# Kernel tuning notes

Hardware: AMD Instinct MI355X
Metric: run time of the kernel (lower is better)

Reference implementation:

```python
import jax, jax.numpy as jnp
import numpy as np

N_NODES = 65536
N_EDGES = 524288
GRAPH_SIZE = 512  # equal-size graphs -> batch = arange(N)//512
N_GRAPHS = N_NODES // GRAPH_SIZE
IN_DIM, HID, OUT_DIM, HEADS = 64, 64, 128, 4


def setup_inputs() -> dict:
    key = jax.random.key(0)
    ks = jax.random.split(key, 24)
    s = 0.1  # init scale
    # within-graph random edges
    g = jax.random.randint(ks[0], (N_EDGES,), 0, N_GRAPHS)
    off = jax.random.randint(ks[1], (2, N_EDGES), 0, GRAPH_SIZE)
    edge_index = (g[None, :] * GRAPH_SIZE + off).astype(jnp.int32)
    batch = (jnp.arange(N_NODES) // GRAPH_SIZE).astype(jnp.int32)
    rn = lambda k, sh: jax.random.normal(k, sh, jnp.float32) * s
    return {
        'x': jax.random.normal(ks[2], (N_NODES, IN_DIM), jnp.float32),
        'edge_index': edge_index, 'batch': batch,
        'W1': rn(ks[3], (IN_DIM, HEADS * HID)), 'a1s': rn(ks[4], (HEADS, HID)),
        'a1d': rn(ks[5], (HEADS, HID)), 'b1': jnp.zeros((HEADS * HID,), jnp.float32),
        'W2': rn(ks[6], (HEADS * HID, HEADS * HID)), 'a2s': rn(ks[7], (HEADS, HID)),
        'a2d': rn(ks[8], (HEADS, HID)), 'b2': jnp.zeros((HEADS * HID,), jnp.float32),
        'W3': rn(ks[9], (HEADS * HID, OUT_DIM)), 'a3s': rn(ks[10], (1, OUT_DIM)),
        'a3d': rn(ks[11], (1, OUT_DIM)), 'b3': jnp.zeros((OUT_DIM,), jnp.float32),
        'g1': jnp.ones((HEADS * HID,), jnp.float32), 'be1': jnp.zeros((HEADS * HID,), jnp.float32),
        'g2': jnp.ones((HEADS * HID,), jnp.float32), 'be2': jnp.zeros((HEADS * HID,), jnp.float32),
        'Wr': rn(ks[12], (IN_DIM, OUT_DIM)), 'br': jnp.zeros((OUT_DIM,), jnp.float32),
        'Wq': rn(ks[13], (OUT_DIM, OUT_DIM)), 'Wk': rn(ks[14], (OUT_DIM, OUT_DIM)),
        'Wv': rn(ks[15], (OUT_DIM, OUT_DIM)), 'Wo': rn(ks[16], (OUT_DIM, OUT_DIM)),
        'bo': jnp.zeros((OUT_DIM,), jnp.float32),
    }


def _gat(x, src, dst, W, a_s, a_d, b, heads, out_ch):
    N = x.shape[0]
    h = (x @ W).reshape(N, heads, out_ch)          # [N,H,C]
    e_s = (h * a_s).sum(-1)                        # [N,H]
    e_d = (h * a_d).sum(-1)
    e = jax.nn.leaky_relu(e_s[src] + e_d[dst], 0.2)  # [E,H]
    m = jax.ops.segment_max(e, dst, num_segments=N)
    p = jnp.exp(e - m[dst])
    z = jax.ops.segment_sum(p, dst, num_segments=N)
    alpha = p / (z[dst] + 1e-16)
    out = jax.ops.segment_sum(alpha[:, :, None] * h[src], dst, num_segments=N)
    return out.reshape(N, heads * out_ch) + b


def _ln(x, g, b):
    mu = x.mean(-1, keepdims=True)
    v = ((x - mu) ** 2).mean(-1, keepdims=True)
    return (x - mu) * jax.lax.rsqrt(v + 1e-5) * g + b


def _mha(x, Wq, Wk, Wv, Wo, bo, heads):
    B, n, D = x.shape
    hd = D // heads
    q = (x @ Wq).reshape(B, n, heads, hd)
    k = (x @ Wk).reshape(B, n, heads, hd)
    v = (x @ Wv).reshape(B, n, heads, hd)
    energy = jnp.einsum('bqhd,bkhd->bhqk', q, k)
    att = jax.nn.softmax(energy / jnp.sqrt(jnp.float32(D)), axis=-1)
    out = jnp.einsum('bhqk,bkhd->bqhd', att, v).reshape(B, n, D)
    return out @ Wo + bo


def reference(x, edge_index, batch, W1, a1s, a1d, b1, W2, a2s, a2d, b2,
              W3, a3s, a3d, b3, g1, be1, g2, be2, Wr, br, Wq, Wk, Wv, Wo, bo):
    N = x.shape[0]
    loops = jnp.arange(N, dtype=edge_index.dtype)
    src = jnp.concatenate([edge_index[0], loops])  # PyG add_self_loops default
    dst = jnp.concatenate([edge_index[1], loops])
    h = jax.nn.elu(_gat(x, src, dst, W1, a1s, a1d, b1, HEADS, HID))
    h = _ln(h, g1, be1)
    h = jax.nn.elu(_gat(h, src, dst, W2, a2s, a2d, b2, HEADS, HID))
    h = _ln(h, g2, be2)
    h = _gat(h, src, dst, W3, a3s, a3d, b3, 1, OUT_DIM)
    h = h + (x @ Wr + br)
    # equal-size graphs: per-graph self-attention via batched reshape
    hg = h.reshape(N_GRAPHS, GRAPH_SIZE, OUT_DIM)
    hg = _mha(hg, Wq, Wk, Wv, Wo, bo, 4)
    return hg.reshape(N, OUT_DIM)
```

## Files before the change

kernel.cpp:

```cpp
#include <hip/hip_runtime.h>
#include <math.h>

#define N_NODES 65536
#define NUM_EDGES 524288
#define E_TOT   (NUM_EDGES + N_NODES)
#define GSZ 512

typedef _Float16 f16x8 __attribute__((ext_vector_type(8)));
typedef _Float16 f16x4 __attribute__((ext_vector_type(4)));
typedef _Float16 f16x2 __attribute__((ext_vector_type(2)));
typedef float    f32x16 __attribute__((ext_vector_type(16)));

__global__ void k_zero_int(int* __restrict__ p, int n) {
  int i = blockIdx.x * blockDim.x + threadIdx.x;
  if (i < n) p[i] = 0;
}

__global__ void k_hist(const int* __restrict__ ei, int* __restrict__ cnt) {
  int e = blockIdx.x * blockDim.x + threadIdx.x;
  if (e >= E_TOT) return;
  int dst = (e < NUM_EDGES) ? ei[NUM_EDGES + e] : (e - NUM_EDGES);
  atomicAdd(&cnt[dst], 1);
}

__global__ void k_scan1(const int* __restrict__ cnt, int* __restrict__ offs,
                        int* __restrict__ sums) {
  __shared__ int s[256];
  int t = threadIdx.x;
  int i = blockIdx.x * 256 + t;
  int v = cnt[i];
  s[t] = v;
  for (int o = 1; o < 256; o <<= 1) {
    __syncthreads();
    int x = (t >= o) ? s[t - o] : 0;
    __syncthreads();
    s[t] += x;
  }
  offs[i] = s[t] - v;
  if (t == 255) sums[blockIdx.x] = s[t];
}

__global__ void k_scan2(int* __restrict__ sums) {
  __shared__ int s[256];
  int t = threadIdx.x;
  int v = sums[t];
  s[t] = v;
  for (int o = 1; o < 256; o <<= 1) {
    __syncthreads();
    int x = (t >= o) ? s[t - o] : 0;
    __syncthreads();
    s[t] += x;
  }
  sums[t] = s[t] - v;
}

__global__ void k_scan3(int* __restrict__ offs, const int* __restrict__ sums,
                        int* __restrict__ cur) {
  int i = blockIdx.x * 256 + threadIdx.x;
  int v = offs[i] + sums[blockIdx.x];
  offs[i] = v;
  cur[i] = v;
  if (i == 0) offs[N_NODES] = E_TOT;
}

__global__ void k_fill(const int* __restrict__ ei, int* __restrict__ cur,
                       int* __restrict__ ssrc) {
  int e = blockIdx.x * blockDim.x + threadIdx.x;
  if (e >= E_TOT) return;
  int src, dst;
  if (e < NUM_EDGES) { src = ei[e]; dst = ei[NUM_EDGES + e]; }
  else               { src = e - NUM_EDGES; dst = src; }
  int pos = atomicAdd(&cur[dst], 1);
  ssrc[pos] = src;
}

__device__ __forceinline__ f16x8 cvt8(float4 a, float4 b) {
  f16x8 h;
  h[0] = (_Float16)a.x; h[1] = (_Float16)a.y;
  h[2] = (_Float16)a.z; h[3] = (_Float16)a.w;
  h[4] = (_Float16)b.x; h[5] = (_Float16)b.y;
  h[6] = (_Float16)b.z; h[7] = (_Float16)b.w;
  return h;
}

#define LDH 40
template <typename TA, typename TC>
__global__ __launch_bounds__(256) void k_gemm(
    const TA* __restrict__ A, const float* __restrict__ B,
    const float* __restrict__ bias, TC* __restrict__ C,
    int M, int N, int K, float cscale) {
  __shared__ __align__(16) _Float16 As[128][LDH];
  __shared__ __align__(16) _Float16 Bs[128][LDH];
  const int t = threadIdx.x;
  const int l = t & 63, w = t >> 6;
  const int m0 = blockIdx.x * 128, n0 = blockIdx.y * 128;
  const int wm = (w >> 1) * 64, wn = (w & 1) * 64;
  const int lm = l & 31, kq = l >> 5;

  f32x16 acc00 = {}, acc01 = {}, acc10 = {}, acc11 = {};

  const int ra = t >> 1, ka = (t & 1) << 4;
  const int nb = (t & 31) << 2, kb = (t >> 5) << 2;

  for (int k0 = 0; k0 < K; k0 += 32) {
    f16x8 a_lo, a_hi;
    if constexpr (sizeof(TA) == 4) {
      const float* ap = (const float*)&A[(size_t)(m0 + ra) * K + k0 + ka];
      float4 av0 = *(const float4*)ap;
      float4 av1 = *(const float4*)(ap + 4);
      float4 av2 = *(const float4*)(ap + 8);
      float4 av3 = *(const float4*)(ap + 12);
      a_lo = cvt8(av0, av1);
      a_hi = cvt8(av2, av3);
    } else {
      const _Float16* ap = (const _Float16*)&A[(size_t)(m0 + ra) * K + k0 + ka];
      a_lo = *(const f16x8*)ap;
      a_hi = *(const f16x8*)(ap + 8);
    }
    const float* bp = &B[(size_t)(k0 + kb) * N + n0 + nb];
    float4 bv0 = *(const float4*)bp;
    float4 bv1 = *(const float4*)(bp + N);
    float4 bv2 = *(const float4*)(bp + 2 * N);
    float4 bv3 = *(const float4*)(bp + 3 * N);
    __syncthreads();
    *(f16x8*)&As[ra][ka]     = a_lo;
    *(f16x8*)&As[ra][ka + 8] = a_hi;
    f16x4 g;
    g[0] = (_Float16)bv0.x; g[1] = (_Float16)bv1.x;
    g[2] = (_Float16)bv2.x; g[3] = (_Float16)bv3.x;
    *(f16x4*)&Bs[nb + 0][kb] = g;
    g[0] = (_Float16)bv0.y; g[1] = (_Float16)bv1.y;
    g[2] = (_Float16)bv2.y; g[3] = (_Float16)bv3.y;
    *(f16x4*)&Bs[nb + 1][kb] = g;
    g[0] = (_Float16)bv0.z; g[1] = (_Float16)bv1.z;
    g[2] = (_Float16)bv2.z; g[3] = (_Float16)bv3.z;
    *(f16x4*)&Bs[nb + 2][kb] = g;
    g[0] = (_Float16)bv0.w; g[1] = (_Float16)bv1.w;
    g[2] = (_Float16)bv2.w; g[3] = (_Float16)bv3.w;
    *(f16x4*)&Bs[nb + 3][kb] = g;
    __syncthreads();
#pragma unroll
    for (int ks = 0; ks < 2; ++ks) {
      f16x8 a0 = *(const f16x8*)&As[wm + lm][ks * 16 + kq * 8];
      f16x8 a1 = *(const f16x8*)&As[wm + 32 + lm][ks * 16 + kq * 8];
      f16x8 b0 = *(const f16x8*)&Bs[wn + lm][ks * 16 + kq * 8];
      f16x8 b1 = *(const f16x8*)&Bs[wn + 32 + lm][ks * 16 + kq * 8];
      acc00 = __builtin_amdgcn_mfma_f32_32x32x16_f16(a0, b0, acc00, 0, 0, 0);
      acc01 = __builtin_amdgcn_mfma_f32_32x32x16_f16(a0, b1, acc01, 0, 0, 0);
      acc10 = __builtin_amdgcn_mfma_f32_32x32x16_f16(a1, b0, acc10, 0, 0, 0);
      acc11 = __builtin_amdgcn_mfma_f32_32x32x16_f16(a1, b1, acc11, 0, 0, 0);
    }
  }

  const int cn = n0 + wn + lm;
  float b0v = 0.f, b1v = 0.f;
  if (bias) { b0v = bias[cn]; b1v = bias[cn + 32]; }
  const int rb = 4 * (l >> 5);
#pragma unroll
  for (int r = 0; r < 16; ++r) {
    int row = m0 + wm + (r & 3) + 8 * (r >> 2) + rb;
    C[(size_t)row * N + cn]             = (TC)((acc00[r] + b0v) * cscale);
    C[(size_t)row * N + cn + 32]        = (TC)((acc01[r] + b1v) * cscale);
    C[(size_t)(row + 32) * N + cn]      = (TC)((acc10[r] + b0v) * cscale);
    C[(size_t)(row + 32) * N + cn + 32] = (TC)((acc11[r] + b1v) * cscale);
  }
}

__global__ void k_scores(const _Float16* __restrict__ h, const float* __restrict__ as_,
                         const float* __restrict__ ad_, float* __restrict__ es,
                         float* __restrict__ ed, int H, int C) {
  int t = blockIdx.x * blockDim.x + threadIdx.x;
  if (t >= N_NODES * H) return;
  int hd = t % H;
  const _Float16* hp = h + (size_t)t * C;
  const float* ap = as_ + hd * C;
  const float* dp = ad_ + hd * C;
  float s = 0.f, d = 0.f;
  for (int c = 0; c < C; c += 8) {
    f16x8 hv = *(const f16x8*)&hp[c];
    float4 a0 = *(const float4*)&ap[c];
    float4 a1 = *(const float4*)&ap[c + 4];
    float4 d0 = *(const float4*)&dp[c];
    float4 d1 = *(const float4*)&dp[c + 4];
    float h0 = (float)hv[0], h1 = (float)hv[1], h2 = (float)hv[2], h3 = (float)hv[3];
    float h4 = (float)hv[4], h5 = (float)hv[5], h6 = (float)hv[6], h7 = (float)hv[7];
    s += h0 * a0.x + h1 * a0.y + h2 * a0.z + h3 * a0.w;
    s += h4 * a1.x + h5 * a1.y + h6 * a1.z + h7 * a1.w;
    d += h0 * d0.x + h1 * d0.y + h2 * d0.z + h3 * d0.w;
    d += h4 * d1.x + h5 * d1.y + h6 * d1.z + h7 * d1.w;
  }
  es[t] = s; ed[t] = d;
}

__device__ __forceinline__ float lrelu02(float e) { return e >= 0.f ? e : 0.2f * e; }

__global__ __launch_bounds__(256) void k_agg256(
    const _Float16* __restrict__ h, const float* __restrict__ es,
    const float* __restrict__ ed, const int* __restrict__ offs,
    const int* __restrict__ ssrc, const float* __restrict__ bias,
    const float* __restrict__ lng, const float* __restrict__ lnb,
    _Float16* __restrict__ out) {
  int lane = threadIdx.x & 63;
  int n = blockIdx.x * 4 + (threadIdx.x >> 6);
  int head = lane >> 4;
  int o0 = offs[n], deg = offs[n + 1] - o0;
  float4 edv = *(const float4*)&ed[n * 4];
  float edh = (head & 2) ? ((head & 1) ? edv.w : edv.z)
                         : ((head & 1) ? edv.y : edv.x);
  float m0 = -1e30f, m1 = -1e30f, m2 = -1e30f, m3 = -1e30f;
  for (int j = lane; j < deg; j += 64) {
    int s = ssrc[o0 + j];
    float4 ev = *(const float4*)&es[s * 4];
    m0 = fmaxf(m0, lrelu02(ev.x + edv.x));
    m1 = fmaxf(m1, lrelu02(ev.y + edv.y));
    m2 = fmaxf(m2, lrelu02(ev.z + edv.z));
    m3 = fmaxf(m3, lrelu02(ev.w + edv.w));
  }
#pragma unroll
  for (int o = 1; o < 64; o <<= 1) {
    m0 = fmaxf(m0, __shfl_xor(m0, o));
    m1 = fmaxf(m1, __shfl_xor(m1, o));
    m2 = fmaxf(m2, __shfl_xor(m2, o));
    m3 = fmaxf(m3, __shfl_xor(m3, o));
  }
  float mh = (head & 2) ? ((head & 1) ? m3 : m2) : ((head & 1) ? m1 : m0);
  float z = 0.f, a0 = 0.f, a1 = 0.f, a2 = 0.f, a3 = 0.f;
  int c0 = lane * 4;
  for (int j = 0; j < deg; ++j) {
    int s = ssrc[o0 + j];
    float p = __expf(lrelu02(es[s * 4 + head] + edh) - mh);
    z += p;
    f16x4 hv = *(const f16x4*)&h[(size_t)s * 256 + c0];
    a0 += p * (float)hv[0]; a1 += p * (float)hv[1];
    a2 += p * (float)hv[2]; a3 += p * (float)hv[3];
  }
  float inv = 1.f / (z + 1e-16f);
  float4 bv = *(const float4*)&bias[c0];
  float v0 = a0 * inv + bv.x; v0 = v0 > 0.f ? v0 : __expf(v0) - 1.f;
  float v1 = a1 * inv + bv.y; v1 = v1 > 0.f ? v1 : __expf(v1) - 1.f;
  float v2 = a2 * inv + bv.z; v2 = v2 > 0.f ? v2 : __expf(v2) - 1.f;
  float v3 = a3 * inv + bv.w; v3 = v3 > 0.f ? v3 : __expf(v3) - 1.f;
  float sum = v0 + v1 + v2 + v3;
#pragma unroll
  for (int o = 1; o < 64; o <<= 1) sum += __shfl_xor(sum, o);
  float mean = sum * (1.f / 256.f);
  float d0 = v0 - mean, d1 = v1 - mean, d2 = v2 - mean, d3 = v3 - mean;
  float sq = d0 * d0 + d1 * d1 + d2 * d2 + d3 * d3;
#pragma unroll
  for (int o = 1; o < 64; o <<= 1) sq += __shfl_xor(sq, o);
  float rs = rsqrtf(sq * (1.f / 256.f) + 1e-5f);
  float4 gv = *(const float4*)&lng[c0];
  float4 ev2 = *(const float4*)&lnb[c0];
  f16x4 o4;
  o4[0] = (_Float16)(d0 * rs * gv.x + ev2.x);
  o4[1] = (_Float16)(d1 * rs * gv.y + ev2.y);
  o4[2] = (_Float16)(d2 * rs * gv.z + ev2.z);
  o4[3] = (_Float16)(d3 * rs * gv.w + ev2.w);
  *(f16x4*)&out[(size_t)n * 256 + c0] = o4;
}

__global__ __launch_bounds__(256) void k_agg128(
    const _Float16* __restrict__ h, const float* __restrict__ es,
    const float* __restrict__ ed, const int* __restrict__ offs,
    const int* __restrict__ ssrc, const float* __restrict__ bias,
    float* __restrict__ io) {
  int lane = threadIdx.x & 63;
  int n = blockIdx.x * 4 + (threadIdx.x >> 6);
  int o0 = offs[n], deg = offs[n + 1] - o0;
  float edv = ed[n];
  float mx = -1e30f;
  for (int j = lane; j < deg; j += 64) {
    int s = ssrc[o0 + j];
    mx = fmaxf(mx, lrelu02(es[s] + edv));
  }
#pragma unroll
  for (int o = 1; o < 64; o <<= 1) mx = fmaxf(mx, __shfl_xor(mx, o));
  float z = 0.f, a0 = 0.f, a1 = 0.f;
  int c0 = lane * 2;
  for (int j = 0; j < deg; ++j) {
    int s = ssrc[o0 + j];
    float p = __expf(lrelu02(es[s] + edv) - mx);
    z += p;
    f16x2 hv = *(const f16x2*)&h[(size_t)s * 128 + c0];
    a0 += p * (float)hv[0]; a1 += p * (float)hv[1];
  }
  float inv = 1.f / (z + 1e-16f);
  float2 r = *(const float2*)&io[(size_t)n * 128 + c0];
  float2 o2;
  o2.x = a0 * inv + bias[c0]     + r.x;
  o2.y = a1 * inv + bias[c0 + 1] + r.y;
  *(float2*)&io[(size_t)n * 128 + c0] = o2;
}

__global__ __launch_bounds__(512) void k_attn(
    const _Float16* __restrict__ Q, const _Float16* __restrict__ K,
    const _Float16* __restrict__ V, _Float16* __restrict__ O) {
  __shared__ __align__(16) _Float16 Ks[64][40];
  __shared__ __align__(16) _Float16 VsT[32][72];
  const int g = blockIdx.x >> 2, hd = blockIdx.x & 3;
  const int t = threadIdx.x;
  const int l = t & 63, w = t >> 6;
  const int h = l >> 5, l31 = l & 31;
  const size_t base = (size_t)g * (GSZ * 128) + hd * 32;

  f16x8 qf[2][2];
#pragma unroll
  for (int j = 0; j < 2; ++j)
#pragma unroll
    for (int ks = 0; ks < 2; ++ks)
      qf[j][ks] = *(const f16x8*)&Q[base + (size_t)(w * 64 + j * 32 + l31) * 128 + ks * 16 + 8 * h];

  f32x16 o0 = {}, o1 = {};
  float la0 = 0.f, la1 = 0.f, m0 = -1e30f, m1 = -1e30f;

  const int kr = t >> 3, dc = (t & 7) * 4;
  for (int kt = 0; kt < GSZ; kt += 64) {
    f16x4 kg = *(const f16x4*)&K[base + (size_t)(kt + kr) * 128 + dc];
    f16x4 vg = *(const f16x4*)&V[base + (size_t)(kt + kr) * 128 + dc];
    __syncthreads();
    *(f16x4*)&Ks[kr][dc] = kg;
    VsT[dc + 0][kr] = vg[0];
    VsT[dc + 1][kr] = vg[1];
    VsT[dc + 2][kr] = vg[2];
    VsT[dc + 3][kr] = vg[3];
    __syncthreads();

#pragma unroll
    for (int s2 = 0; s2 < 2; ++s2) {
      f16x8 ka0 = *(const f16x8*)&Ks[s2 * 32 + l31][8 * h];
      f16x8 ka1 = *(const f16x8*)&Ks[s2 * 32 + l31][16 + 8 * h];
      f16x8 va0 = *(const f16x8*)&VsT[l31][s2 * 32 + 8 * h];
      f16x8 va1 = *(const f16x8*)&VsT[l31][s2 * 32 + 16 + 8 * h];
#pragma unroll
      for (int j = 0; j < 2; ++j) {
        f32x16 s = {};
        s = __builtin_amdgcn_mfma_f32_32x32x16_f16(ka0, qf[j][0], s, 0, 0, 0);
        s = __builtin_amdgcn_mfma_f32_32x32x16_f16(ka1, qf[j][1], s, 0, 0, 0);
        float tm = s[0];
#pragma unroll
        for (int r = 1; r < 16; ++r) tm = fmaxf(tm, s[r]);
        tm = fmaxf(tm, __shfl_xor(tm, 32));
        float* mj = j ? &m1 : &m0;
        float* lj = j ? &la1 : &la0;
        f32x16* oj = j ? &o1 : &o0;
        if (tm > *mj + 10.f) {
          float sc = exp2f(*mj - tm);
          *lj *= sc;
#pragma unroll
          for (int r = 0; r < 16; ++r) (*oj)[r] *= sc;
          *mj = tm;
        }
        float p[16]; float ls = 0.f;
#pragma unroll
        for (int r = 0; r < 16; ++r) { p[r] = exp2f(s[r] - *mj); ls += p[r]; }
        *lj += ls;
#pragma unroll
        for (int kk = 0; kk < 2; ++kk) {
          const int rb = kk * 8;
          unsigned a01 = __builtin_bit_cast(unsigned, __builtin_amdgcn_cvt_pkrtz(p[rb + 0], p[rb + 1]));
          unsigned a23 = __builtin_bit_cast(unsigned, __builtin_amdgcn_cvt_pkrtz(p[rb + 2], p[rb + 3]));
          unsigned b01 = __builtin_bit_cast(unsigned, __builtin_amdgcn_cvt_pkrtz(p[rb + 4], p[rb + 5]));
          unsigned b23 = __builtin_bit_cast(unsigned, __builtin_amdgcn_cvt_pkrtz(p[rb + 6], p[rb + 7]));
          unsigned sa01 = (unsigned)__shfl_xor((int)a01, 32);
          unsigned sa23 = (unsigned)__shfl_xor((int)a23, 32);
          unsigned sb01 = (unsigned)__shfl_xor((int)b01, 32);
          unsigned sb23 = (unsigned)__shfl_xor((int)b23, 32);
          union { unsigned u[4]; f16x8 v; } pb;
          pb.u[0] = h ? sb01 : a01;
          pb.u[1] = h ? sb23 : a23;
          pb.u[2] = h ? b01 : sa01;
          pb.u[3] = h ? b23 : sa23;
          *oj = __builtin_amdgcn_mfma_f32_32x32x16_f16(kk ? va1 : va0, pb.v, *oj, 0, 0, 0);
        }
      }
    }
  }

  la0 += __shfl_xor(la0, 32);
  la1 += __shfl_xor(la1, 32);
  const float i0 = 1.f / la0, i1 = 1.f / la1;
#pragma unroll
  for (int r = 0; r < 16; ++r) {
    int dv = (r & 3) + 8 * (r >> 2) + 4 * h;
    O[base + (size_t)(w * 64 + l31) * 128 + dv]      = (_Float16)(o0[r] * i0);
    O[base + (size_t)(w * 64 + 32 + l31) * 128 + dv] = (_Float16)(o1[r] * i1);
  }
}

extern "C" void kernel_launch(void* const* d_in, const int* in_sizes, int n_in,
                              void* d_out, int out_size, void* d_ws, size_t ws_size,
                              hipStream_t stream) {
  (void)in_sizes; (void)n_in; (void)out_size; (void)ws_size;
  const float* x   = (const float*)d_in[0];
  const int*   ei  = (const int*)d_in[1];
  const float* W1  = (const float*)d_in[3];
  const float* a1s = (const float*)d_in[4];
  const float* a1d = (const float*)d_in[5];
  const float* b1  = (const float*)d_in[6];
  const float* W2  = (const float*)d_in[7];
  const float* a2s = (const float*)d_in[8];
  const float* a2d = (const float*)d_in[9];
  const float* b2  = (const float*)d_in[10];
  const float* W3  = (const float*)d_in[11];
  const float* a3s = (const float*)d_in[12];
  const float* a3d = (const float*)d_in[13];
  const float* b3  = (const float*)d_in[14];
  const float* g1  = (const float*)d_in[15];
  const float* be1 = (const float*)d_in[16];
  const float* g2  = (const float*)d_in[17];
  const float* be2 = (const float*)d_in[18];
  const float* Wr  = (const float*)d_in[19];
  const float* br  = (const float*)d_in[20];
  const float* Wq  = (const float*)d_in[21];
  const float* Wk  = (const float*)d_in[22];
  const float* Wv  = (const float*)d_in[23];
  const float* Wo  = (const float*)d_in[24];
  const float* bo  = (const float*)d_in[25];
  float* out = (float*)d_out;

  _Float16* Hbuf = (_Float16*)d_ws;
  _Float16* Abuf = Hbuf + (size_t)N_NODES * 256;
  float* esb = (float*)(Abuf + (size_t)N_NODES * 256);
  float* edb = esb + (size_t)N_NODES * 4;
  int* offs = (int*)(edb + (size_t)N_NODES * 4);
  int* cur  = offs + N_NODES + 4;
  int* ssrc = cur + N_NODES;
  int* sums = ssrc + E_TOT;

  dim3 blk(256), blk512(512);
  k_zero_int<<<256, blk, 0, stream>>>(cur, N_NODES);
  k_hist<<<(E_TOT + 255) / 256, blk, 0, stream>>>(ei, cur);
  k_scan1<<<256, blk, 0, stream>>>(cur, offs, sums);
  k_scan2<<<1, blk, 0, stream>>>(sums);
  k_scan3<<<256, blk, 0, stream>>>(offs, sums, cur);
  k_fill<<<(E_TOT + 255) / 256, blk, 0, stream>>>(ei, cur, ssrc);

  dim3 gN128(512, 1), gN256(512, 2);
  const float qsc = 0.0883883476483184f * 1.44269504088896f;

  k_gemm<float, float><<<gN128, blk, 0, stream>>>(x, Wr, br, out, N_NODES, 128, 64, 1.f);

  k_gemm<float, _Float16><<<gN256, blk, 0, stream>>>(x, W1, nullptr, Hbuf, N_NODES, 256, 64, 1.f);
  k_scores<<<N_NODES * 4 / 256, blk, 0, stream>>>(Hbuf, a1s, a1d, esb, edb, 4, 64);
  k_agg256<<<N_NODES / 4, blk, 0, stream>>>(Hbuf, esb, edb, offs, ssrc, b1, g1, be1, Abuf);
  k_gemm<_Float16, _Float16><<<gN256, blk, 0, stream>>>(Abuf, W2, nullptr, Hbuf, N_NODES, 256, 256, 1.f);
  k_scores<<<N_NODES * 4 / 256, blk, 0, stream>>>(Hbuf, a2s, a2d, esb, edb, 4, 64);
  k_agg256<<<N_NODES / 4, blk, 0, stream>>>(Hbuf, esb, edb, offs, ssrc, b2, g2, be2, Abuf);
  k_gemm<_Float16, _Float16><<<gN128, blk, 0, stream>>>(Abuf, W3, nullptr, Hbuf, N_NODES, 128, 256, 1.f);
  k_scores<<<N_NODES / 256, blk, 0, stream>>>(Hbuf, a3s, a3d, esb, edb, 1, 128);
  k_agg128<<<N_NODES / 4, blk, 0, stream>>>(Hbuf, esb, edb, offs, ssrc, b3, out);

  _Float16* Qb  = Abuf;
  _Float16* Kb  = Abuf + (size_t)N_NODES * 128;
  _Float16* Vb  = Hbuf;
  _Float16* AOb = Hbuf + (size_t)N_NODES * 128;
  k_gemm<float, _Float16><<<gN128, blk, 0, stream>>>(out, Wq, nullptr, Qb, N_NODES, 128, 128, qsc);
  k_gemm<float, _Float16><<<gN128, blk, 0, stream>>>(out, Wk, nullptr, Kb, N_NODES, 128, 128, 1.f);
  k_gemm<float, _Float16><<<gN128, blk, 0, stream>>>(out, Wv, nullptr, Vb, N_NODES, 128, 128, 1.f);
  k_attn<<<512, blk512, 0, stream>>>(Qb, Kb, Vb, AOb);
  k_gemm<_Float16, float><<<gN128, blk, 0, stream>>>(AOb, Wo, bo, out, N_NODES, 128, 128, 1.f);
}
```

Measured before the change: 630.3 us.

## Drop segment-max pass in GAT aggregation, unroll edge loop, swizzle block order

Removes the max-subtraction pre-pass in both aggregation kernels and instead clamps logits at 80 before exponentiation. This saves a full pass over neighbour scores and a wave reduction per node. The edge loop is also unrolled by two to get more loads in flight, and block indices are swizzled across groups of 8 to change which nodes run concurrently. Without max subtraction the softmax can lose precision or saturate when logits are large, and the clamp only keeps it finite.

```diff
diff --git a/kernel.cpp b/kernel.cpp
--- a/kernel.cpp
+++ b/kernel.cpp
@@ -201,38 +201,36 @@
     const float* __restrict__ lng, const float* __restrict__ lnb,
     _Float16* __restrict__ out) {
   int lane = threadIdx.x & 63;
-  int n = blockIdx.x * 4 + (threadIdx.x >> 6);
+  int bid = blockIdx.x;
+  int swz = (bid & 7) * ((int)gridDim.x >> 3) + (bid >> 3);
+  int n = swz * 4 + (threadIdx.x >> 6);
   int head = lane >> 4;
   int o0 = offs[n], deg = offs[n + 1] - o0;
   float4 edv = *(const float4*)&ed[n * 4];
   float edh = (head & 2) ? ((head & 1) ? edv.w : edv.z)
                          : ((head & 1) ? edv.y : edv.x);
-  float m0 = -1e30f, m1 = -1e30f, m2 = -1e30f, m3 = -1e30f;
-  for (int j = lane; j < deg; j += 64) {
-    int s = ssrc[o0 + j];
-    float4 ev = *(const float4*)&es[s * 4];
-    m0 = fmaxf(m0, lrelu02(ev.x + edv.x));
-    m1 = fmaxf(m1, lrelu02(ev.y + edv.y));
-    m2 = fmaxf(m2, lrelu02(ev.z + edv.z));
-    m3 = fmaxf(m3, lrelu02(ev.w + edv.w));
-  }
-#pragma unroll
-  for (int o = 1; o < 64; o <<= 1) {
-    m0 = fmaxf(m0, __shfl_xor(m0, o));
-    m1 = fmaxf(m1, __shfl_xor(m1, o));
-    m2 = fmaxf(m2, __shfl_xor(m2, o));
-    m3 = fmaxf(m3, __shfl_xor(m3, o));
-  }
-  float mh = (head & 2) ? ((head & 1) ? m3 : m2) : ((head & 1) ? m1 : m0);
   float z = 0.f, a0 = 0.f, a1 = 0.f, a2 = 0.f, a3 = 0.f;
   int c0 = lane * 4;
-  for (int j = 0; j < deg; ++j) {
-    int s = ssrc[o0 + j];
-    float p = __expf(lrelu02(es[s * 4 + head] + edh) - mh);
-    z += p;
-    f16x4 hv = *(const f16x4*)&h[(size_t)s * 256 + c0];
-    a0 += p * (float)hv[0]; a1 += p * (float)hv[1];
-    a2 += p * (float)hv[2]; a3 += p * (float)hv[3];
+  int j = 0;
+  for (; j + 2 <= deg; j += 2) {
+    int s0 = ssrc[o0 + j], s1 = ssrc[o0 + j + 1];
+    float p0 = __expf(fminf(lrelu02(es[s0 * 4 + head] + edh), 80.f));
+    float p1 = __expf(fminf(lrelu02(es[s1 * 4 + head] + edh), 80.f));
+    f16x4 h0 = *(const f16x4*)&h[(size_t)s0 * 256 + c0];
+    f16x4 h1 = *(const f16x4*)&h[(size_t)s1 * 256 + c0];
+    z += p0 + p1;
+    a0 += p0 * (float)h0[0] + p1 * (float)h1[0];
+    a1 += p0 * (float)h0[1] + p1 * (float)h1[1];
+    a2 += p0 * (float)h0[2] + p1 * (float)h1[2];
+    a3 += p0 * (float)h0[3] + p1 * (float)h1[3];
+  }
+  if (j < deg) {
+    int s0 = ssrc[o0 + j];
+    float p0 = __expf(fminf(lrelu02(es[s0 * 4 + head] + edh), 80.f));
+    f16x4 h0 = *(const f16x4*)&h[(size_t)s0 * 256 + c0];
+    z += p0;
+    a0 += p0 * (float)h0[0]; a1 += p0 * (float)h0[1];
+    a2 += p0 * (float)h0[2]; a3 += p0 * (float)h0[3];
   }
   float inv = 1.f / (z + 1e-16f);
   float4 bv = *(const float4*)&bias[c0];
@@ -265,24 +263,30 @@
     const int* __restrict__ ssrc, const float* __restrict__ bias,
     float* __restrict__ io) {
   int lane = threadIdx.x & 63;
-  int n = blockIdx.x * 4 + (threadIdx.x >> 6);
+  int bid = blockIdx.x;
+  int swz = (bid & 7) * ((int)gridDim.x >> 3) + (bid >> 3);
+  int n = swz * 4 + (threadIdx.x >> 6);
   int o0 = offs[n], deg = offs[n + 1] - o0;
   float edv = ed[n];
-  float mx = -1e30f;
-  for (int j = lane; j < deg; j += 64) {
-    int s = ssrc[o0 + j];
-    mx = fmaxf(mx, lrelu02(es[s] + edv));
-  }
-#pragma unroll
-  for (int o = 1; o < 64; o <<= 1) mx = fmaxf(mx, __shfl_xor(mx, o));
   float z = 0.f, a0 = 0.f, a1 = 0.f;
   int c0 = lane * 2;
-  for (int j = 0; j < deg; ++j) {
-    int s = ssrc[o0 + j];
-    float p = __expf(lrelu02(es[s] + edv) - mx);
-    z += p;
-    f16x2 hv = *(const f16x2*)&h[(size_t)s * 128 + c0];
-    a0 += p * (float)hv[0]; a1 += p * (float)hv[1];
+  int j = 0;
+  for (; j + 2 <= deg; j += 2) {
+    int s0 = ssrc[o0 + j], s1 = ssrc[o0 + j + 1];
+    float p0 = __expf(fminf(lrelu02(es[s0] + edv), 80.f));
+    float p1 = __expf(fminf(lrelu02(es[s1] + edv), 80.f));
+    f16x2 h0 = *(const f16x2*)&h[(size_t)s0 * 128 + c0];
+    f16x2 h1 = *(const f16x2*)&h[(size_t)s1 * 128 + c0];
+    z += p0 + p1;
+    a0 += p0 * (float)h0[0] + p1 * (float)h1[0];
+    a1 += p0 * (float)h0[1] + p1 * (float)h1[1];
+  }
+  if (j < deg) {
+    int s0 = ssrc[o0 + j];
+    float p0 = __expf(fminf(lrelu02(es[s0] + edv), 80.f));
+    f16x2 h0 = *(const f16x2*)&h[(size_t)s0 * 128 + c0];
+    z += p0;
+    a0 += p0 * (float)h0[0]; a1 += p0 * (float)h0[1];
   }
   float inv = 1.f / (z + 1e-16f);
   float2 r = *(const float2*)&io[(size_t)n * 128 + c0];
```

Result: faster. 534.9 us (-15.1%).
